# Performance work log

Hardware: AMD Instinct MI355X
Metric: run time of the kernel (lower is better)

## Reference

```python
import jax, jax.numpy as jnp
import numpy as np

N_WAY, N_SHOT = 10, 15
N_QUERY, D = 8192, 1024
C_REG = 0.1
MAX_ITER = 15


def setup_inputs() -> dict:
    key = jax.random.key(0)
    k1, k2 = jax.random.split(key)
    n_sup = N_WAY * N_SHOT
    feat = jax.random.normal(k1, (n_sup + N_QUERY, D), dtype=jnp.float32) * 0.1
    label_support = jnp.arange(N_WAY, dtype=jnp.int32)
    label_query = jax.random.randint(k2, (N_QUERY,), 0, N_WAY, dtype=jnp.int32)
    scale = jnp.ones((1,), dtype=jnp.float32)
    return {"feat": feat, "label_support": label_support,
            "label_query": label_query, "scale": scale}


def _qp_solve(Q, p, h, A):
    """min 0.5 z'Qz + p'z  s.t.  z <= h,  A z = 0.
    Infeasible-start primal-dual interior-point method, MAX_ITER fixed iterations
    (mirrors qpth's QPFunction(maxIter=15) iterative batched-solve structure)."""
    n = Q.shape[0]
    m = A.shape[0]
    dtype = Q.dtype
    z = h - 1.0                      # slack s = h - z = 1 > 0
    s = jnp.ones((n,), dtype)
    lam = jnp.ones((n,), dtype)
    nu = jnp.zeros((m,), dtype)
    sigma = jnp.asarray(0.1, dtype)  # centering parameter

    def step(carry, _):
        z, s, lam, nu = carry
        mu = jnp.dot(s, lam) / n
        rd = Q @ z + p + lam + A.T @ nu      # dual residual
        rp = A @ z                           # primal (equality) residual, b = 0
        rc = s * lam - sigma * mu            # complementarity residual
        r1 = -rd + rc / s
        H = Q + jnp.diag(lam / s)
        L = jnp.linalg.cholesky(H)
        solveH = lambda r: jax.scipy.linalg.cho_solve((L, True), r)
        Hinv_AT = solveH(A.T)                # (n, m)
        Hinv_r1 = solveH(r1)                 # (n,)
        S = A @ Hinv_AT                      # (m, m) Schur complement
        dnu = jnp.linalg.solve(S, A @ Hinv_r1 + rp)
        dz = Hinv_r1 - Hinv_AT @ dnu
        ds = -dz
        dlam = (lam * dz - rc) / s

        def max_step(v, dv):                 # largest alpha keeping v + alpha*dv > 0
            ratios = jnp.where(dv < 0, -v / jnp.where(dv < 0, dv, -1.0), jnp.inf)
            return jnp.min(ratios)

        alpha = jnp.minimum(1.0, 0.99 * jnp.minimum(max_step(s, ds), max_step(lam, dlam)))
        return (z + alpha * dz, s + alpha * ds, lam + alpha * dlam, nu + alpha * dnu), None

    (z, s, lam, nu), _ = jax.lax.scan(step, (z, s, lam, nu), None, length=MAX_ITER)
    return z


def reference(feat, label_support, label_query, scale):
    n_way, n_shot = N_WAY, N_SHOT
    n_sup = n_way * n_shot
    support = feat[:n_sup]                       # (n_sup, d)
    query = feat[n_sup:]                         # (n_q, d)
    sup_labels = jnp.repeat(label_support, n_shot)   # label[0].repeat_interleave(n_shot)

    K = support @ support.T                      # Gram matrix (n_sup, n_sup)
    n = n_sup * n_way
    eye_w = jnp.eye(n_way, dtype=K.dtype)
    # batched_kronecker(K, I_way): index (i*n_way + a)
    Q = jnp.einsum('ij,ab->iajb', K, eye_w).reshape(n, n) + 10.0 * jnp.eye(n, dtype=K.dtype)
    y_onehot = jax.nn.one_hot(sup_labels, n_way, dtype=K.dtype).reshape(n)
    p = -y_onehot                                # e
    h = C_REG * y_onehot                         # box: z <= C_reg * Y (C = I)
    # A = kron(I_{n_sup}, ones(1, n_way))
    A = jnp.einsum('ij,a->ija', jnp.eye(n_sup, dtype=K.dtype),
                   jnp.ones((n_way,), K.dtype)).reshape(n_sup, n)

    qp_sol = _qp_solve(Q, p, h, A).reshape(n_sup, n_way)

    compat = support @ query.T                   # (n_sup, n_q)
    # logits[q, w] = sum_s compat[s, q] * qp_sol[s, w]
    logits = scale[0] * jnp.einsum('sq,sw->qw', compat, qp_sol)
    log_prb = jax.nn.log_softmax(logits, axis=1)     # (n_q, n_way)
    y_q = jax.nn.one_hot(label_query, n_way, dtype=log_prb.dtype)
    loss = -(y_q * log_prb).sum(axis=1).mean()
    return (log_prb, loss)
```

## Files before the change

kernel.cpp:

```cpp
#include <hip/hip_runtime.h>


#define NW    10
#define NSH   15
#define NSUP  150
#define NQ    8192
#define DIM   1024
#define NVAR  1500
#define NP    152
#define NTT   19
#define NACT  (NTT*NTT)
#define TPB   384
#define SIGMA 0.1f
#define PSTR  68

#define OFF_K     0
#define OFF_Z     22800
#define OFF_S     24300
#define OFF_LAM   25800
#define OFF_NU    27300
#define OFF_R1    27452
#define OFF_DZ    28952
#define OFF_DLAM  30452
#define OFF_DNU   31952
#define OFF_RP    32104
#define OFF_MU    32256
#define OFF_ALPHA 32257
#define OFF_LP    32260
#define OFF_WT    34308
#define OFF_G     44548
#define OFF_SMAT  46048
#define OFF_X     69152
#define XSZ       (NP*NP)

__device__ __forceinline__ void bgj_invert(float (&H)[8][8], const int t, const int tr, const int tc,
                                           float (*rowbuf)[PSTR], float (*colbuf)[PSTR],
                                           float (*wbuf)[PSTR], float* pivinv) {
  const bool act = (t < NACT);
  const int r8 = t & 7;
  const int wj = t >> 3;
  for (int kb = 0; kb < NTT; ++kb) {
    if (act && tr == kb) {
      float4* dst = (float4*)(&rowbuf[tc][0]);
#pragma unroll
      for (int r = 0; r < 8; ++r) {
        dst[2*r]   = make_float4(H[r][0],H[r][1],H[r][2],H[r][3]);
        dst[2*r+1] = make_float4(H[r][4],H[r][5],H[r][6],H[r][7]);
      }
    }
    if (act && tc == kb) {
      float4* dst = (float4*)(&colbuf[tr][0]);
#pragma unroll
      for (int r = 0; r < 8; ++r) {
        dst[2*r]   = make_float4(H[r][0],H[r][1],H[r][2],H[r][3]);
        dst[2*r+1] = make_float4(H[r][4],H[r][5],H[r][6],H[r][7]);
      }
    }
    __syncthreads();
    if (t < 64) {
      const int r = t >> 3, c = t & 7;
      float p = rowbuf[kb][t];
#pragma unroll
      for (int pp = 0; pp < 8; ++pp) {
        const float pv   = __shfl(p, pp*9, 64);
        const float d    = 1.0f / pv;
        const float rowv = __shfl(p, pp*8 + c, 64);
        const float colv = __shfl(p, r*8 + pp, 64);
        const float nr   = rowv * d;
        float v = fmaf(-colv, nr, p);
        if (r == pp) v = nr;
        if (c == pp) v = -colv * d;
        if (r == pp && c == pp) v = d;
        p = v;
      }
      pivinv[t] = p;
    }
    __syncthreads();
    if (t < 8*NTT) {
      float w[8];
      if (wj == kb) {
#pragma unroll
        for (int c = 0; c < 8; ++c) w[c] = pivinv[r8*8+c];
      } else {
        const float4* rs = (const float4*)(&rowbuf[wj][0]);
#pragma unroll
        for (int c = 0; c < 8; ++c) w[c] = 0.0f;
#pragma unroll
        for (int q = 0; q < 8; ++q) {
          const float pq = pivinv[r8*8+q];
          const float4 x = rs[2*q], y = rs[2*q+1];
          w[0]=fmaf(pq,x.x,w[0]); w[1]=fmaf(pq,x.y,w[1]); w[2]=fmaf(pq,x.z,w[2]); w[3]=fmaf(pq,x.w,w[3]);
          w[4]=fmaf(pq,y.x,w[4]); w[5]=fmaf(pq,y.y,w[5]); w[6]=fmaf(pq,y.z,w[6]); w[7]=fmaf(pq,y.w,w[7]);
        }
      }
      float4* wd = (float4*)(&wbuf[wj][0]);
      wd[2*r8]   = make_float4(w[0],w[1],w[2],w[3]);
      wd[2*r8+1] = make_float4(w[4],w[5],w[6],w[7]);
    }
    __syncthreads();
    if (act) {
      if (tr == kb) {
        const float4* wsrc = (const float4*)(&wbuf[tc][0]);
#pragma unroll
        for (int r = 0; r < 8; ++r) {
          const float4 x = wsrc[2*r], y = wsrc[2*r+1];
          H[r][0]=x.x; H[r][1]=x.y; H[r][2]=x.z; H[r][3]=x.w;
          H[r][4]=y.x; H[r][5]=y.y; H[r][6]=y.z; H[r][7]=y.w;
        }
      } else {
        float C[8][8];
        const float4* cs = (const float4*)(&colbuf[tr][0]);
#pragma unroll
        for (int r = 0; r < 8; ++r) {
          const float4 x = cs[2*r], y = cs[2*r+1];
          C[r][0]=x.x; C[r][1]=x.y; C[r][2]=x.z; C[r][3]=x.w;
          C[r][4]=y.x; C[r][5]=y.y; C[r][6]=y.z; C[r][7]=y.w;
        }
        if (tc == kb) {
#pragma unroll
          for (int r = 0; r < 8; ++r)
#pragma unroll
            for (int c = 0; c < 8; ++c) H[r][c] = 0.0f;
        }
        const float4* wsrc = (const float4*)(&wbuf[tc][0]);
#pragma unroll
        for (int q = 0; q < 8; ++q) {
          const float4 x = wsrc[2*q], y = wsrc[2*q+1];
          const float w0=x.x,w1=x.y,w2=x.z,w3=x.w,w4=y.x,w5=y.y,w6=y.z,w7=y.w;
#pragma unroll
          for (int r = 0; r < 8; ++r) {
            const float cq = C[r][q];
            H[r][0]=fmaf(-cq,w0,H[r][0]); H[r][1]=fmaf(-cq,w1,H[r][1]);
            H[r][2]=fmaf(-cq,w2,H[r][2]); H[r][3]=fmaf(-cq,w3,H[r][3]);
            H[r][4]=fmaf(-cq,w4,H[r][4]); H[r][5]=fmaf(-cq,w5,H[r][5]);
            H[r][6]=fmaf(-cq,w6,H[r][6]); H[r][7]=fmaf(-cq,w7,H[r][7]);
          }
        }
      }
    }
    __syncthreads();
  }
}

__global__ __launch_bounds__(256) void k_gram(const float* __restrict__ feat, float* __restrict__ ws) {
  const int bi = blockIdx.x / 10, bj = blockIdx.x % 10;
  const int t = threadIdx.x;
  const int r = t / 15, c = t % 15;
  const bool act = (t < 225);
  __shared__ float As[15][65], Bs[15][65];
  float acc = 0.0f;
  for (int ch = 0; ch < 16; ++ch) {
    for (int idx = t; idx < 960; idx += 256) {
      const int rr = idx >> 6, dd = idx & 63;
      As[rr][dd] = feat[(bi*15+rr)*DIM + ch*64 + dd];
      Bs[rr][dd] = feat[(bj*15+rr)*DIM + ch*64 + dd];
    }
    __syncthreads();
    if (act) {
      for (int dd = 0; dd < 64; ++dd) acc += As[r][dd] * Bs[c][dd];
    }
    __syncthreads();
  }
  if (act) ws[OFF_K + (bi*15+r)*NP + (bj*15+c)] = acc;
}

__global__ __launch_bounds__(1024) void kinit(const int* __restrict__ labSup, float* __restrict__ ws) {
  const int t = threadIdx.x;
  for (int idx = t; idx < NVAR; idx += 1024) {
    const int i = idx / NW, aa = idx % NW;
    const float y = (labSup[i/NSH] == aa) ? 1.0f : 0.0f;
    ws[OFF_Z+idx]   = 0.1f*y - 1.0f;
    ws[OFF_S+idx]   = 1.0f;
    ws[OFF_LAM+idx] = 1.0f;
  }
  if (t < NP) ws[OFF_NU + t] = 0.0f;
  if (t == 0) ws[OFF_MU] = 1.0f;
  if (t < NSUP) {
    float rpv = 0.0f;
    for (int aa = 0; aa < NW; ++aa) {
      const float y = (labSup[t/NSH] == aa) ? 1.0f : 0.0f;
      rpv += 0.1f*y - 1.0f;
    }
    ws[OFF_RP + t] = rpv;
  }
}

__global__ __launch_bounds__(TPB, 2) void kqp1(const int* __restrict__ labSup, float* __restrict__ ws) {
  const int a = blockIdx.x;
  const int t = threadIdx.x;
  const int tr = t / NTT, tc = t % NTT;
  const bool act = (t < NACT);
  __shared__ __align__(16) float rowbuf[NTT][PSTR], colbuf[NTT][PSTR], wbuf[NTT][PSTR];
  __shared__ __align__(16) float pivinv[64];
  __shared__ float zloc[NP], dloc[NP], r1loc[NP];
  __shared__ float pacc[NP][NTT];
  const float mu = ws[OFF_MU];
  for (int i = t; i < NP; i += TPB) {
    if (i < NSUP) {
      zloc[i] = ws[OFF_Z + i*NW + a];
      dloc[i] = ws[OFF_LAM + i*NW + a] / ws[OFF_S + i*NW + a];
    } else { zloc[i] = 0.0f; dloc[i] = 0.0f; }
  }
  __syncthreads();
  float H[8][8];
  if (act) {
#pragma unroll
    for (int r = 0; r < 8; ++r) {
      const int row = 8*tr + r;
      if (row < NSUP) {
        const float4* ks = (const float4*)(ws + OFF_K + row*NP + 8*tc);
        const float4 x = ks[0], y = ks[1];
        H[r][0]=x.x; H[r][1]=x.y; H[r][2]=x.z; H[r][3]=x.w;
        H[r][4]=y.x; H[r][5]=y.y; H[r][6]=y.z; H[r][7]=y.w;
        if (tc == NTT-1) { H[r][6] = 0.0f; H[r][7] = 0.0f; }
      } else {
#pragma unroll
        for (int c = 0; c < 8; ++c) H[r][c] = 0.0f;
      }
#pragma unroll
      for (int c = 0; c < 8; ++c) {
        const int col = 8*tc + c;
        if (col == row) H[r][c] += (row < NSUP) ? (10.0f + dloc[row]) : 1.0f;
      }
    }
#pragma unroll
    for (int r = 0; r < 8; ++r) {
      float p = 0.0f;
#pragma unroll
      for (int c = 0; c < 8; ++c) p = fmaf(H[r][c], zloc[8*tc + c], p);
      pacc[8*tr + r][tc] = p;
    }
  }
  __syncthreads();
  if (t < NSUP) {
    float hz = 0.0f;
    for (int q = 0; q < NTT; ++q) hz += pacc[t][q];
    const float qz  = hz - dloc[t]*zloc[t];
    const float y   = (labSup[t/NSH] == a) ? 1.0f : 0.0f;
    const float svv = ws[OFF_S + t*NW+a], lvv = ws[OFF_LAM + t*NW+a];
    const float rd  = qz - y + lvv + ws[OFF_NU + t];
    const float rc  = svv*lvv - SIGMA*mu;
    const float r1v = -rd + rc/svv;
    ws[OFF_R1 + t*NW+a] = r1v;
    r1loc[t] = r1v;
  }
  if (t >= NSUP && t < NP) r1loc[t] = 0.0f;
  bgj_invert(H, t, tr, tc, rowbuf, colbuf, wbuf, pivinv);
  if (act) {
    float* Xa = ws + OFF_X + a*XSZ;
#pragma unroll
    for (int r = 0; r < 8; ++r) {
      float4* dst = (float4*)(Xa + (8*tr+r)*NP + 8*tc);
      dst[0] = make_float4(H[r][0],H[r][1],H[r][2],H[r][3]);
      dst[1] = make_float4(H[r][4],H[r][5],H[r][6],H[r][7]);
    }
#pragma unroll
    for (int r = 0; r < 8; ++r) {
      float p = 0.0f;
#pragma unroll
      for (int c = 0; c < 8; ++c) p = fmaf(H[r][c], r1loc[8*tc+c], p);
      pacc[8*tr+r][tc] = p;
    }
  }
  __syncthreads();
  if (t < NSUP) {
    float g = 0.0f;
    for (int q = 0; q < NTT; ++q) g += pacc[t][q];
    ws[OFF_G + t*NW + a] = g;
  }
}

__global__ __launch_bounds__(256) void k_sum(float* __restrict__ ws) {
  for (int idx = blockIdx.x*256 + threadIdx.x; idx < XSZ; idx += gridDim.x*256) {
    float v = 0.0f;
#pragma unroll
    for (int a = 0; a < NW; ++a) v += ws[OFF_X + a*XSZ + idx];
    ws[OFF_SMAT + idx] = v;
  }
}

__global__ __launch_bounds__(TPB, 2) void kqp2(float* __restrict__ ws) {
  const int t = threadIdx.x;
  const int tr = t / NTT, tc = t % NTT;
  const bool act = (t < NACT);
  __shared__ __align__(16) float rowbuf[NTT][PSTR], colbuf[NTT][PSTR], wbuf[NTT][PSTR];
  __shared__ __align__(16) float pivinv[64];
  __shared__ float tloc[NP];
  __shared__ float pacc[NP][NTT];
  float Sg[8][8];
  if (act) {
#pragma unroll
    for (int r = 0; r < 8; ++r) {
      const float4* ss = (const float4*)(ws + OFF_SMAT + (8*tr+r)*NP + 8*tc);
      const float4 x = ss[0], y = ss[1];
      Sg[r][0]=x.x; Sg[r][1]=x.y; Sg[r][2]=x.z; Sg[r][3]=x.w;
      Sg[r][4]=y.x; Sg[r][5]=y.y; Sg[r][6]=y.z; Sg[r][7]=y.w;
    }
  }
  if (t < NP) {
    float v = 0.0f;
    if (t < NSUP) {
      v = ws[OFF_RP + t];
#pragma unroll
      for (int a = 0; a < NW; ++a) v += ws[OFF_G + t*NW + a];
    }
    tloc[t] = v;
  }
  bgj_invert(Sg, t, tr, tc, rowbuf, colbuf, wbuf, pivinv);
  if (act) {
#pragma unroll
    for (int r = 0; r < 8; ++r) {
      float p = 0.0f;
#pragma unroll
      for (int c = 0; c < 8; ++c) p = fmaf(Sg[r][c], tloc[8*tc+c], p);
      pacc[8*tr+r][tc] = p;
    }
  }
  __syncthreads();
  if (t < NP) {
    float v = 0.0f;
    if (t < NSUP) for (int q = 0; q < NTT; ++q) v += pacc[t][q];
    ws[OFF_DNU + t] = v;
  }
  if (t == 0) ((unsigned*)ws)[OFF_ALPHA] = 0x7F800000u;
}

__global__ __launch_bounds__(TPB) void kqp3(float* __restrict__ ws) {
  const int a = blockIdx.x;
  const int t = threadIdx.x;
  const int tr = t / NTT, tc = t % NTT;
  const bool act = (t < NACT);
  __shared__ float vloc[NP];
  __shared__ float pacc[NP][NTT];
  const float mu = ws[OFF_MU];
  for (int i = t; i < NP; i += TPB)
    vloc[i] = (i < NSUP) ? (ws[OFF_R1 + i*NW + a] - ws[OFF_DNU + i]) : 0.0f;
  __syncthreads();
  if (act) {
    const float* Xa = ws + OFF_X + a*XSZ;
    const int cb = 8*tc;
#pragma unroll
    for (int r = 0; r < 8; ++r) {
      const float4* src = (const float4*)(Xa + (8*tr+r)*NP + cb);
      const float4 v0 = src[0], v1 = src[1];
      pacc[8*tr+r][tc] =
          v0.x*vloc[cb+0] + v0.y*vloc[cb+1] + v0.z*vloc[cb+2] + v0.w*vloc[cb+3]
        + v1.x*vloc[cb+4] + v1.y*vloc[cb+5] + v1.z*vloc[cb+6] + v1.w*vloc[cb+7];
    }
  }
  __syncthreads();
  if (t < NSUP) {
    float dzv = 0.0f;
    for (int q = 0; q < NTT; ++q) dzv += pacc[t][q];
    const float svv = ws[OFF_S + t*NW+a], lvv = ws[OFF_LAM + t*NW+a];
    const float rc  = svv*lvv - SIGMA*mu;
    const float dlv = (lvv*dzv - rc)/svv;
    ws[OFF_DZ + t*NW+a]   = dzv;
    ws[OFF_DLAM + t*NW+a] = dlv;
    unsigned* slot = (unsigned*)(ws) + OFF_ALPHA;
    const float dsv = -dzv;
    if (dsv < 0.0f) atomicMin(slot, __float_as_uint(-svv/dsv));
    if (dlv < 0.0f) atomicMin(slot, __float_as_uint(-lvv/dlv));
  }
}

__global__ __launch_bounds__(1024) void kqp4(float* __restrict__ ws) {
  const int t = threadIdx.x;
  __shared__ float zsh[NVAR];
  __shared__ float red[1024];
  const float am = __uint_as_float(((unsigned*)ws)[OFF_ALPHA]);
  const float alpha = fminf(1.0f, 0.99f * am);
  float part = 0.0f;
  for (int idx = t; idx < NVAR; idx += 1024) {
    const float dzv = ws[OFF_DZ + idx], dlv = ws[OFF_DLAM + idx];
    const float zn = ws[OFF_Z + idx]   + alpha*dzv;
    const float sn = ws[OFF_S + idx]   - alpha*dzv;
    const float ln = ws[OFF_LAM + idx] + alpha*dlv;
    ws[OFF_Z+idx]=zn; ws[OFF_S+idx]=sn; ws[OFF_LAM+idx]=ln;
    zsh[idx] = zn;
    part += sn*ln;
  }
  if (t < NSUP) ws[OFF_NU + t] += alpha * ws[OFF_DNU + t];
  red[t] = part;
  __syncthreads();
  for (int off = 512; off > 0; off >>= 1) {
    if (t < off) red[t] += red[t + off];
    __syncthreads();
  }
  if (t == 0) ws[OFF_MU] = red[0] / (float)NVAR;
  if (t < NSUP) {
    float rpv = 0.0f;
#pragma unroll
    for (int a = 0; a < NW; ++a) rpv += zsh[t*NW+a];
    ws[OFF_RP + t] = rpv;
  }
}

__global__ __launch_bounds__(1024) void k_wt(const float* __restrict__ feat,
                                             const float* __restrict__ scale,
                                             float* __restrict__ ws) {
  const int w = blockIdx.x;
  const int dd = threadIdx.x;
  float acc = 0.0f;
  for (int ss = 0; ss < NSUP; ++ss)
    acc += feat[ss*DIM + dd] * ws[OFF_Z + ss*NW + w];
  ws[OFF_WT + w*DIM + dd] = acc * scale[0];
}

__global__ __launch_bounds__(256) void k_logits(const float* __restrict__ feat,
                                                const int* __restrict__ labq,
                                                float* __restrict__ out,
                                                float* __restrict__ ws) {
  const int t = threadIdx.x;
  const int wv = t >> 6, l = t & 63;
  const int q = blockIdx.x*4 + wv;
  __shared__ float wtl[NW][DIM];
  __shared__ float lpart[4];
  for (int idx = t; idx < NW*DIM; idx += 256) wtl[idx >> 10][idx & 1023] = ws[OFF_WT + idx];
  __syncthreads();
  const float* qrow = feat + (size_t)(NSUP + q)*DIM;
  float acc[NW];
#pragma unroll
  for (int w = 0; w < NW; ++w) acc[w] = 0.0f;
#pragma unroll
  for (int c = 0; c < 4; ++c) {
    const float4 qv = *(const float4*)(qrow + c*256 + 4*l);
#pragma unroll
    for (int w = 0; w < NW; ++w) {
      const float4 wvv = *(const float4*)(&wtl[w][c*256 + 4*l]);
      acc[w] += qv.x*wvv.x + qv.y*wvv.y + qv.z*wvv.z + qv.w*wvv.w;
    }
  }
#pragma unroll
  for (int w = 0; w < NW; ++w) {
#pragma unroll
    for (int off = 32; off > 0; off >>= 1)
      acc[w] += __shfl_xor(acc[w], off, 64);
  }
  float m = acc[0];
#pragma unroll
  for (int w = 1; w < NW; ++w) m = fmaxf(m, acc[w]);
  float se = 0.0f;
#pragma unroll
  for (int w = 0; w < NW; ++w) se += expf(acc[w]-m);
  const float lse = m + logf(se);
  const int y = labq[q];
  if (l == 0) {
    float lpy = 0.0f;
#pragma unroll
    for (int w = 0; w < NW; ++w) {
      const float lp = acc[w] - lse;
      out[q*NW + w] = lp;
      if (w == y) lpy = lp;
    }
    lpart[wv] = -lpy;
  }
  __syncthreads();
  if (t == 0) ws[OFF_LP + blockIdx.x] = lpart[0]+lpart[1]+lpart[2]+lpart[3];
}

__global__ __launch_bounds__(1024) void k_loss(float* __restrict__ out, const float* __restrict__ ws) {
  const int t = threadIdx.x;
  __shared__ float red[1024];
  red[t] = ws[OFF_LP + t] + ws[OFF_LP + 1024 + t];
  __syncthreads();
  for (int off = 512; off > 0; off >>= 1) {
    if (t < off) red[t] += red[t + off];
    __syncthreads();
  }
  if (t == 0) out[NQ*NW] = red[0] / (float)NQ;
}

extern "C" void kernel_launch(void* const* d_in, const int* in_sizes, int n_in,
                              void* d_out, int out_size, void* d_ws, size_t ws_size,
                              hipStream_t stream) {
  const float* feat  = (const float*)d_in[0];
  const int*   labS  = (const int*)d_in[1];
  const int*   labQ  = (const int*)d_in[2];
  const float* scale = (const float*)d_in[3];
  float* ws  = (float*)d_ws;
  float* out = (float*)d_out;

  k_gram<<<100, 256, 0, stream>>>(feat, ws);
  kinit<<<1, 1024, 0, stream>>>(labS, ws);
  for (int it = 0; it < 15; ++it) {
    kqp1<<<NW, TPB, 0, stream>>>(labS, ws);
    k_sum<<<32, 256, 0, stream>>>(ws);
    kqp2<<<1,  TPB, 0, stream>>>(ws);
    kqp3<<<NW, TPB, 0, stream>>>(ws);
    kqp4<<<1, 1024, 0, stream>>>(ws);
  }
  k_wt<<<NW, 1024, 0, stream>>>(feat, scale, ws);
  k_logits<<<NQ/4, 256, 0, stream>>>(feat, labQ, out, ws);
  k_loss<<<1, 1024, 0, stream>>>(out, ws);
}
```

Measured before the change: 2.167 ms.

## Fuse QP solve steps into one kernel and cut barriers in block inversion

The per-iteration kernels kqp2, kqp3 and kqp4 are merged into a single one-block kernel. It computes dnu, loops over the ten classes to form dz and dlam, takes alpha through a shared-memory atomic min, and applies the update with a wave-shuffle reduction. This removes two launches per iteration, 30 in total. The block Gauss-Jordan inversion is restructured so every wave redundantly inverts the pivot block via shuffles, and the next pivot row and column are staged at the end of the current step into a double-buffered colbuf. That cuts the barriers per pivot step from four to two. The trade-off is that kqp3's ten-block parallel work now runs serially in one block.

```diff
diff --git a/kernel.cpp b/kernel.cpp
--- a/kernel.cpp
+++ b/kernel.cpp
@@ -22,10 +22,8 @@
 #define OFF_R1    27452
 #define OFF_DZ    28952
 #define OFF_DLAM  30452
-#define OFF_DNU   31952
 #define OFF_RP    32104
 #define OFF_MU    32256
-#define OFF_ALPHA 32257
 #define OFF_LP    32260
 #define OFF_WT    34308
 #define OFF_G     44548
@@ -33,69 +31,51 @@
 #define OFF_X     69152
 #define XSZ       (NP*NP)
 
-__device__ __forceinline__ void bgj_invert(float (&H)[8][8], const int t, const int tr, const int tc,
-                                           float (*rowbuf)[PSTR], float (*colbuf)[PSTR],
-                                           float (*wbuf)[PSTR], float* pivinv) {
+__device__ __forceinline__ void bgj_core(float (&H)[8][8], const int t, const int tr, const int tc,
+                                         float (*rowbuf)[PSTR], float (*colbuf)[NTT][PSTR],
+                                         float (*wbuf)[PSTR]) {
+  const int lane = t & 63;
+  const int pr = lane >> 3, pc = lane & 7;
+  const int r8 = t & 7;
+  const int wj2 = t >> 3;
+  const int jb = wj2 >> 1;
+  const int jh4 = (wj2 & 1) << 2;
+  const bool wact = (t < 8*NTT*2);
   const bool act = (t < NACT);
-  const int r8 = t & 7;
-  const int wj = t >> 3;
   for (int kb = 0; kb < NTT; ++kb) {
-    if (act && tr == kb) {
-      float4* dst = (float4*)(&rowbuf[tc][0]);
-#pragma unroll
-      for (int r = 0; r < 8; ++r) {
-        dst[2*r]   = make_float4(H[r][0],H[r][1],H[r][2],H[r][3]);
-        dst[2*r+1] = make_float4(H[r][4],H[r][5],H[r][6],H[r][7]);
-      }
-    }
-    if (act && tc == kb) {
-      float4* dst = (float4*)(&colbuf[tr][0]);
-#pragma unroll
-      for (int r = 0; r < 8; ++r) {
-        dst[2*r]   = make_float4(H[r][0],H[r][1],H[r][2],H[r][3]);
-        dst[2*r+1] = make_float4(H[r][4],H[r][5],H[r][6],H[r][7]);
-      }
-    }
-    __syncthreads();
-    if (t < 64) {
-      const int r = t >> 3, c = t & 7;
-      float p = rowbuf[kb][t];
-#pragma unroll
-      for (int pp = 0; pp < 8; ++pp) {
-        const float pv   = __shfl(p, pp*9, 64);
-        const float d    = 1.0f / pv;
-        const float rowv = __shfl(p, pp*8 + c, 64);
-        const float colv = __shfl(p, r*8 + pp, 64);
-        const float nr   = rowv * d;
-        float v = fmaf(-colv, nr, p);
-        if (r == pp) v = nr;
-        if (c == pp) v = -colv * d;
-        if (r == pp && c == pp) v = d;
-        p = v;
-      }
-      pivinv[t] = p;
-    }
-    __syncthreads();
-    if (t < 8*NTT) {
-      float w[8];
-      if (wj == kb) {
-#pragma unroll
-        for (int c = 0; c < 8; ++c) w[c] = pivinv[r8*8+c];
+    const int cur = kb & 1, nxt = cur ^ 1;
+    float p = rowbuf[kb][lane];
+#pragma unroll
+    for (int pp = 0; pp < 8; ++pp) {
+      const float pv   = __shfl(p, pp*9, 64);
+      const float d    = 1.0f / pv;
+      const float rowv = __shfl(p, pp*8 + pc, 64);
+      const float colv = __shfl(p, pr*8 + pp, 64);
+      const float nr   = rowv * d;
+      float v = fmaf(-colv, nr, p);
+      if (pr == pp) v = nr;
+      if (pc == pp) v = -colv * d;
+      if (pr == pp && pc == pp) v = d;
+      p = v;
+    }
+    float pv8[8];
+#pragma unroll
+    for (int q = 0; q < 8; ++q) pv8[q] = __shfl(p, r8*8 + q, 64);
+    if (wact) {
+      float w0, w1, w2, w3;
+      if (jb == kb) {
+        w0 = jh4 ? pv8[4] : pv8[0]; w1 = jh4 ? pv8[5] : pv8[1];
+        w2 = jh4 ? pv8[6] : pv8[2]; w3 = jh4 ? pv8[7] : pv8[3];
       } else {
-        const float4* rs = (const float4*)(&rowbuf[wj][0]);
-#pragma unroll
-        for (int c = 0; c < 8; ++c) w[c] = 0.0f;
+        w0 = w1 = w2 = w3 = 0.0f;
 #pragma unroll
         for (int q = 0; q < 8; ++q) {
-          const float pq = pivinv[r8*8+q];
-          const float4 x = rs[2*q], y = rs[2*q+1];
-          w[0]=fmaf(pq,x.x,w[0]); w[1]=fmaf(pq,x.y,w[1]); w[2]=fmaf(pq,x.z,w[2]); w[3]=fmaf(pq,x.w,w[3]);
-          w[4]=fmaf(pq,y.x,w[4]); w[5]=fmaf(pq,y.y,w[5]); w[6]=fmaf(pq,y.z,w[6]); w[7]=fmaf(pq,y.w,w[7]);
-        }
-      }
-      float4* wd = (float4*)(&wbuf[wj][0]);
-      wd[2*r8]   = make_float4(w[0],w[1],w[2],w[3]);
-      wd[2*r8+1] = make_float4(w[4],w[5],w[6],w[7]);
+          const float4 x = *(const float4*)(&rowbuf[jb][q*8 + jh4]);
+          w0 = fmaf(pv8[q], x.x, w0); w1 = fmaf(pv8[q], x.y, w1);
+          w2 = fmaf(pv8[q], x.z, w2); w3 = fmaf(pv8[q], x.w, w3);
+        }
+      }
+      *(float4*)(&wbuf[jb][r8*8 + jh4]) = make_float4(w0, w1, w2, w3);
     }
     __syncthreads();
     if (act) {
@@ -109,7 +89,7 @@
         }
       } else {
         float C[8][8];
-        const float4* cs = (const float4*)(&colbuf[tr][0]);
+        const float4* cs = (const float4*)(&colbuf[cur][tr][0]);
 #pragma unroll
         for (int r = 0; r < 8; ++r) {
           const float4 x = cs[2*r], y = cs[2*r+1];
@@ -134,6 +114,24 @@
             H[r][2]=fmaf(-cq,w2,H[r][2]); H[r][3]=fmaf(-cq,w3,H[r][3]);
             H[r][4]=fmaf(-cq,w4,H[r][4]); H[r][5]=fmaf(-cq,w5,H[r][5]);
             H[r][6]=fmaf(-cq,w6,H[r][6]); H[r][7]=fmaf(-cq,w7,H[r][7]);
+          }
+        }
+      }
+      if (kb < NTT-1) {
+        if (tr == kb+1) {
+          float4* dst = (float4*)(&rowbuf[tc][0]);
+#pragma unroll
+          for (int r = 0; r < 8; ++r) {
+            dst[2*r]   = make_float4(H[r][0],H[r][1],H[r][2],H[r][3]);
+            dst[2*r+1] = make_float4(H[r][4],H[r][5],H[r][6],H[r][7]);
+          }
+        }
+        if (tc == kb+1) {
+          float4* dst = (float4*)(&colbuf[nxt][tr][0]);
+#pragma unroll
+          for (int r = 0; r < 8; ++r) {
+            dst[2*r]   = make_float4(H[r][0],H[r][1],H[r][2],H[r][3]);
+            dst[2*r+1] = make_float4(H[r][4],H[r][5],H[r][6],H[r][7]);
           }
         }
       }
@@ -185,13 +183,12 @@
   }
 }
 
-__global__ __launch_bounds__(TPB, 2) void kqp1(const int* __restrict__ labSup, float* __restrict__ ws) {
+__global__ __launch_bounds__(TPB, 2) void kqpA(const int* __restrict__ labSup, float* __restrict__ ws) {
   const int a = blockIdx.x;
   const int t = threadIdx.x;
   const int tr = t / NTT, tc = t % NTT;
   const bool act = (t < NACT);
-  __shared__ __align__(16) float rowbuf[NTT][PSTR], colbuf[NTT][PSTR], wbuf[NTT][PSTR];
-  __shared__ __align__(16) float pivinv[64];
+  __shared__ __align__(16) float rowbuf[NTT][PSTR], colbuf[2][NTT][PSTR], wbuf[NTT][PSTR];
   __shared__ float zloc[NP], dloc[NP], r1loc[NP];
   __shared__ float pacc[NP][NTT];
   const float mu = ws[OFF_MU];
@@ -229,6 +226,22 @@
 #pragma unroll
       for (int c = 0; c < 8; ++c) p = fmaf(H[r][c], zloc[8*tc + c], p);
       pacc[8*tr + r][tc] = p;
+    }
+    if (tr == 0) {
+      float4* dst = (float4*)(&rowbuf[tc][0]);
+#pragma unroll
+      for (int r = 0; r < 8; ++r) {
+        dst[2*r]   = make_float4(H[r][0],H[r][1],H[r][2],H[r][3]);
+        dst[2*r+1] = make_float4(H[r][4],H[r][5],H[r][6],H[r][7]);
+      }
+    }
+    if (tc == 0) {
+      float4* dst = (float4*)(&colbuf[0][tr][0]);
+#pragma unroll
+      for (int r = 0; r < 8; ++r) {
+        dst[2*r]   = make_float4(H[r][0],H[r][1],H[r][2],H[r][3]);
+        dst[2*r+1] = make_float4(H[r][4],H[r][5],H[r][6],H[r][7]);
+      }
     }
   }
   __syncthreads();
@@ -243,9 +256,8 @@
     const float r1v = -rd + rc/svv;
     ws[OFF_R1 + t*NW+a] = r1v;
     r1loc[t] = r1v;
-  }
-  if (t >= NSUP && t < NP) r1loc[t] = 0.0f;
-  bgj_invert(H, t, tr, tc, rowbuf, colbuf, wbuf, pivinv);
+  } else if (t < NP) r1loc[t] = 0.0f;
+  bgj_core(H, t, tr, tc, rowbuf, colbuf, wbuf);
   if (act) {
     float* Xa = ws + OFF_X + a*XSZ;
 #pragma unroll
@@ -279,14 +291,27 @@
   }
 }
 
-__global__ __launch_bounds__(TPB, 2) void kqp2(float* __restrict__ ws) {
+__global__ __launch_bounds__(TPB, 2) void kqpB(float* __restrict__ ws) {
   const int t = threadIdx.x;
   const int tr = t / NTT, tc = t % NTT;
   const bool act = (t < NACT);
-  __shared__ __align__(16) float rowbuf[NTT][PSTR], colbuf[NTT][PSTR], wbuf[NTT][PSTR];
-  __shared__ __align__(16) float pivinv[64];
-  __shared__ float tloc[NP];
+  __shared__ __align__(16) float rowbuf[NTT][PSTR], colbuf[2][NTT][PSTR], wbuf[NTT][PSTR];
+  __shared__ float tloc[NP], dnuloc[NP], vloc[NP];
   __shared__ float pacc[NP][NTT];
+  __shared__ float zsh[NVAR];
+  __shared__ float wred[TPB/64];
+  __shared__ unsigned alphaU;
+  const float mu = ws[OFF_MU];
+  if (t == 0) alphaU = 0x7F800000u;
+  if (t < NP) {
+    float v = 0.0f;
+    if (t < NSUP) {
+      v = ws[OFF_RP + t];
+#pragma unroll
+      for (int a = 0; a < NW; ++a) v += ws[OFF_G + t*NW + a];
+    }
+    tloc[t] = v;
+  }
   float Sg[8][8];
   if (act) {
 #pragma unroll
@@ -296,17 +321,25 @@
       Sg[r][0]=x.x; Sg[r][1]=x.y; Sg[r][2]=x.z; Sg[r][3]=x.w;
       Sg[r][4]=y.x; Sg[r][5]=y.y; Sg[r][6]=y.z; Sg[r][7]=y.w;
     }
-  }
-  if (t < NP) {
-    float v = 0.0f;
-    if (t < NSUP) {
-      v = ws[OFF_RP + t];
-#pragma unroll
-      for (int a = 0; a < NW; ++a) v += ws[OFF_G + t*NW + a];
-    }
-    tloc[t] = v;
-  }
-  bgj_invert(Sg, t, tr, tc, rowbuf, colbuf, wbuf, pivinv);
+    if (tr == 0) {
+      float4* dst = (float4*)(&rowbuf[tc][0]);
+#pragma unroll
+      for (int r = 0; r < 8; ++r) {
+        dst[2*r]   = make_float4(Sg[r][0],Sg[r][1],Sg[r][2],Sg[r][3]);
+        dst[2*r+1] = make_float4(Sg[r][4],Sg[r][5],Sg[r][6],Sg[r][7]);
+      }
+    }
+    if (tc == 0) {
+      float4* dst = (float4*)(&colbuf[0][tr][0]);
+#pragma unroll
+      for (int r = 0; r < 8; ++r) {
+        dst[2*r]   = make_float4(Sg[r][0],Sg[r][1],Sg[r][2],Sg[r][3]);
+        dst[2*r+1] = make_float4(Sg[r][4],Sg[r][5],Sg[r][6],Sg[r][7]);
+      }
+    }
+  }
+  __syncthreads();
+  bgj_core(Sg, t, tr, tc, rowbuf, colbuf, wbuf);
   if (act) {
 #pragma unroll
     for (int r = 0; r < 8; ++r) {
@@ -320,58 +353,43 @@
   if (t < NP) {
     float v = 0.0f;
     if (t < NSUP) for (int q = 0; q < NTT; ++q) v += pacc[t][q];
-    ws[OFF_DNU + t] = v;
-  }
-  if (t == 0) ((unsigned*)ws)[OFF_ALPHA] = 0x7F800000u;
-}
-
-__global__ __launch_bounds__(TPB) void kqp3(float* __restrict__ ws) {
-  const int a = blockIdx.x;
-  const int t = threadIdx.x;
-  const int tr = t / NTT, tc = t % NTT;
-  const bool act = (t < NACT);
-  __shared__ float vloc[NP];
-  __shared__ float pacc[NP][NTT];
-  const float mu = ws[OFF_MU];
-  for (int i = t; i < NP; i += TPB)
-    vloc[i] = (i < NSUP) ? (ws[OFF_R1 + i*NW + a] - ws[OFF_DNU + i]) : 0.0f;
-  __syncthreads();
-  if (act) {
-    const float* Xa = ws + OFF_X + a*XSZ;
-    const int cb = 8*tc;
-#pragma unroll
-    for (int r = 0; r < 8; ++r) {
-      const float4* src = (const float4*)(Xa + (8*tr+r)*NP + cb);
-      const float4 v0 = src[0], v1 = src[1];
-      pacc[8*tr+r][tc] =
-          v0.x*vloc[cb+0] + v0.y*vloc[cb+1] + v0.z*vloc[cb+2] + v0.w*vloc[cb+3]
-        + v1.x*vloc[cb+4] + v1.y*vloc[cb+5] + v1.z*vloc[cb+6] + v1.w*vloc[cb+7];
-    }
-  }
-  __syncthreads();
-  if (t < NSUP) {
-    float dzv = 0.0f;
-    for (int q = 0; q < NTT; ++q) dzv += pacc[t][q];
-    const float svv = ws[OFF_S + t*NW+a], lvv = ws[OFF_LAM + t*NW+a];
-    const float rc  = svv*lvv - SIGMA*mu;
-    const float dlv = (lvv*dzv - rc)/svv;
-    ws[OFF_DZ + t*NW+a]   = dzv;
-    ws[OFF_DLAM + t*NW+a] = dlv;
-    unsigned* slot = (unsigned*)(ws) + OFF_ALPHA;
-    const float dsv = -dzv;
-    if (dsv < 0.0f) atomicMin(slot, __float_as_uint(-svv/dsv));
-    if (dlv < 0.0f) atomicMin(slot, __float_as_uint(-lvv/dlv));
-  }
-}
-
-__global__ __launch_bounds__(1024) void kqp4(float* __restrict__ ws) {
-  const int t = threadIdx.x;
-  __shared__ float zsh[NVAR];
-  __shared__ float red[1024];
-  const float am = __uint_as_float(((unsigned*)ws)[OFF_ALPHA]);
-  const float alpha = fminf(1.0f, 0.99f * am);
+    dnuloc[t] = v;
+  }
+  __syncthreads();
+  for (int a = 0; a < NW; ++a) {
+    for (int i = t; i < NP; i += TPB)
+      vloc[i] = (i < NSUP) ? (ws[OFF_R1 + i*NW + a] - dnuloc[i]) : 0.0f;
+    __syncthreads();
+    if (act) {
+      const float* Xa = ws + OFF_X + a*XSZ;
+      const int cb = 8*tc;
+#pragma unroll
+      for (int r = 0; r < 8; ++r) {
+        const float4* src = (const float4*)(Xa + (8*tr+r)*NP + cb);
+        const float4 v0 = src[0], v1 = src[1];
+        pacc[8*tr+r][tc] =
+            v0.x*vloc[cb+0] + v0.y*vloc[cb+1] + v0.z*vloc[cb+2] + v0.w*vloc[cb+3]
+          + v1.x*vloc[cb+4] + v1.y*vloc[cb+5] + v1.z*vloc[cb+6] + v1.w*vloc[cb+7];
+      }
+    }
+    __syncthreads();
+    if (t < NSUP) {
+      float dzv = 0.0f;
+      for (int q = 0; q < NTT; ++q) dzv += pacc[t][q];
+      const float svv = ws[OFF_S + t*NW+a], lvv = ws[OFF_LAM + t*NW+a];
+      const float rc  = svv*lvv - SIGMA*mu;
+      const float dlv = (lvv*dzv - rc)/svv;
+      ws[OFF_DZ + t*NW+a]   = dzv;
+      ws[OFF_DLAM + t*NW+a] = dlv;
+      const float dsv = -dzv;
+      if (dsv < 0.0f) atomicMin(&alphaU, __float_as_uint(-svv/dsv));
+      if (dlv < 0.0f) atomicMin(&alphaU, __float_as_uint(-lvv/dlv));
+    }
+    __syncthreads();
+  }
+  const float alpha = fminf(1.0f, 0.99f * __uint_as_float(alphaU));
   float part = 0.0f;
-  for (int idx = t; idx < NVAR; idx += 1024) {
+  for (int idx = t; idx < NVAR; idx += TPB) {
     const float dzv = ws[OFF_DZ + idx], dlv = ws[OFF_DLAM + idx];
     const float zn = ws[OFF_Z + idx]   + alpha*dzv;
     const float sn = ws[OFF_S + idx]   - alpha*dzv;
@@ -380,14 +398,17 @@
     zsh[idx] = zn;
     part += sn*ln;
   }
-  if (t < NSUP) ws[OFF_NU + t] += alpha * ws[OFF_DNU + t];
-  red[t] = part;
-  __syncthreads();
-  for (int off = 512; off > 0; off >>= 1) {
-    if (t < off) red[t] += red[t + off];
-    __syncthreads();
-  }
-  if (t == 0) ws[OFF_MU] = red[0] / (float)NVAR;
+  if (t < NSUP) ws[OFF_NU + t] += alpha * dnuloc[t];
+#pragma unroll
+  for (int off = 32; off > 0; off >>= 1) part += __shfl_xor(part, off, 64);
+  if ((t & 63) == 0) wred[t >> 6] = part;
+  __syncthreads();
+  if (t == 0) {
+    float s = 0.0f;
+#pragma unroll
+    for (int wv = 0; wv < TPB/64; ++wv) s += wred[wv];
+    ws[OFF_MU] = s / (float)NVAR;
+  }
   if (t < NSUP) {
     float rpv = 0.0f;
 #pragma unroll
@@ -484,11 +505,9 @@
   k_gram<<<100, 256, 0, stream>>>(feat, ws);
   kinit<<<1, 1024, 0, stream>>>(labS, ws);
   for (int it = 0; it < 15; ++it) {
-    kqp1<<<NW, TPB, 0, stream>>>(labS, ws);
+    kqpA<<<NW, TPB, 0, stream>>>(labS, ws);
     k_sum<<<32, 256, 0, stream>>>(ws);
-    kqp2<<<1,  TPB, 0, stream>>>(ws);
-    kqp3<<<NW, TPB, 0, stream>>>(ws);
-    kqp4<<<1, 1024, 0, stream>>>(ws);
+    kqpB<<<1, TPB, 0, stream>>>(ws);
   }
   k_wt<<<NW, 1024, 0, stream>>>(feat, scale, ws);
   k_logits<<<NQ/4, 256, 0, stream>>>(feat, labQ, out, ws);
```

Result: slower. 2.818 ms (+30.0%).

## Rework block Gauss-Jordan inversion to 4x8 tiles with double-buffered panels

Applied to the files above, without the earlier changes.

Splits the 152x152 inversion across 722 threads holding 4x8 register tiles instead of 361 threads holding 8x8, doubling the threads per block. Each wave now recomputes the 8x8 pivot inverse redundantly via shuffles, removing the shared pivinv buffer and one barrier per step. The next step's pivot row and column panels are written at the end of each step, with the column panel stored transposed and double-buffered, cutting the barriers per step from four to two. The cost is higher per-thread redundant pivot work and more shared-memory traffic per FMA in the smaller tiles.

```diff
diff --git a/kernel.cpp b/kernel.cpp
--- a/kernel.cpp
+++ b/kernel.cpp
@@ -8,11 +8,16 @@
 #define DIM   1024
 #define NVAR  1500
 #define NP    152
+#define CB    19
+#define RB    38
+#define NACT2 722
+#define TPB2  768
+#define TPB   384
 #define NTT   19
 #define NACT  (NTT*NTT)
-#define TPB   384
 #define SIGMA 0.1f
 #define PSTR  68
+#define CTSTR 36
 
 #define OFF_K     0
 #define OFF_Z     22800
@@ -33,108 +38,95 @@
 #define OFF_X     69152
 #define XSZ       (NP*NP)
 
-__device__ __forceinline__ void bgj_invert(float (&H)[8][8], const int t, const int tr, const int tc,
-                                           float (*rowbuf)[PSTR], float (*colbuf)[PSTR],
-                                           float (*wbuf)[PSTR], float* pivinv) {
-  const bool act = (t < NACT);
-  const int r8 = t & 7;
-  const int wj = t >> 3;
-  for (int kb = 0; kb < NTT; ++kb) {
-    if (act && tr == kb) {
-      float4* dst = (float4*)(&rowbuf[tc][0]);
-#pragma unroll
-      for (int r = 0; r < 8; ++r) {
-        dst[2*r]   = make_float4(H[r][0],H[r][1],H[r][2],H[r][3]);
-        dst[2*r+1] = make_float4(H[r][4],H[r][5],H[r][6],H[r][7]);
-      }
-    }
-    if (act && tc == kb) {
-      float4* dst = (float4*)(&colbuf[tr][0]);
-#pragma unroll
-      for (int r = 0; r < 8; ++r) {
-        dst[2*r]   = make_float4(H[r][0],H[r][1],H[r][2],H[r][3]);
-        dst[2*r+1] = make_float4(H[r][4],H[r][5],H[r][6],H[r][7]);
-      }
-    }
-    __syncthreads();
-    if (t < 64) {
-      const int r = t >> 3, c = t & 7;
-      float p = rowbuf[kb][t];
-#pragma unroll
-      for (int pp = 0; pp < 8; ++pp) {
-        const float pv   = __shfl(p, pp*9, 64);
-        const float d    = 1.0f / pv;
-        const float rowv = __shfl(p, pp*8 + c, 64);
-        const float colv = __shfl(p, r*8 + pp, 64);
-        const float nr   = rowv * d;
-        float v = fmaf(-colv, nr, p);
-        if (r == pp) v = nr;
-        if (c == pp) v = -colv * d;
-        if (r == pp && c == pp) v = d;
-        p = v;
-      }
-      pivinv[t] = p;
-    }
-    __syncthreads();
-    if (t < 8*NTT) {
-      float w[8];
-      if (wj == kb) {
-#pragma unroll
-        for (int c = 0; c < 8; ++c) w[c] = pivinv[r8*8+c];
-      } else {
-        const float4* rs = (const float4*)(&rowbuf[wj][0]);
-#pragma unroll
-        for (int c = 0; c < 8; ++c) w[c] = 0.0f;
+__device__ __forceinline__ void bgj48(float (&H)[4][8], const int t, const int trb, const int tcb,
+                                      float (*rowbuf)[PSTR], float (*colbufT)[RB][CTSTR],
+                                      float (*wbuf)[PSTR]) {
+  const int lane = t & 63;
+  const int pr = lane >> 3, pc = lane & 7;
+  const int wr  = t & 7;
+  const int wcp = t >> 3;
+  const int wcb = wcp >> 2;
+  const int wc2 = (wcp & 3) * 2;
+  const bool wact = (t < 608);
+  const bool act  = (t < NACT2);
+  for (int kb = 0; kb < CB; ++kb) {
+    const int cur = kb & 1, nxt = cur ^ 1;
+    float p = rowbuf[kb][lane];
+#pragma unroll
+    for (int pp = 0; pp < 8; ++pp) {
+      const float pv   = __shfl(p, pp*9, 64);
+      const float d    = 1.0f / pv;
+      const float rowv = __shfl(p, pp*8 + pc, 64);
+      const float colv = __shfl(p, pr*8 + pp, 64);
+      const float nr   = rowv * d;
+      float v = fmaf(-colv, nr, p);
+      if (pr == pp) v = nr;
+      if (pc == pp) v = -colv * d;
+      if (pr == pp && pc == pp) v = d;
+      p = v;
+    }
+    float pv8[8];
+#pragma unroll
+    for (int q = 0; q < 8; ++q) pv8[q] = __shfl(p, wr*8 + q, 64);
+    if (wact) {
+      float w0, w1;
+      if (wcb == kb) { w0 = pv8[wc2]; w1 = pv8[wc2+1]; }
+      else {
+        w0 = w1 = 0.0f;
 #pragma unroll
         for (int q = 0; q < 8; ++q) {
-          const float pq = pivinv[r8*8+q];
-          const float4 x = rs[2*q], y = rs[2*q+1];
-          w[0]=fmaf(pq,x.x,w[0]); w[1]=fmaf(pq,x.y,w[1]); w[2]=fmaf(pq,x.z,w[2]); w[3]=fmaf(pq,x.w,w[3]);
-          w[4]=fmaf(pq,y.x,w[4]); w[5]=fmaf(pq,y.y,w[5]); w[6]=fmaf(pq,y.z,w[6]); w[7]=fmaf(pq,y.w,w[7]);
+          const float2 rv = *(const float2*)(&rowbuf[wcb][q*8 + wc2]);
+          w0 = fmaf(pv8[q], rv.x, w0);
+          w1 = fmaf(pv8[q], rv.y, w1);
         }
       }
-      float4* wd = (float4*)(&wbuf[wj][0]);
-      wd[2*r8]   = make_float4(w[0],w[1],w[2],w[3]);
-      wd[2*r8+1] = make_float4(w[4],w[5],w[6],w[7]);
+      *(float2*)(&wbuf[wcb][wr*8 + wc2]) = make_float2(w0, w1);
     }
     __syncthreads();
     if (act) {
-      if (tr == kb) {
-        const float4* wsrc = (const float4*)(&wbuf[tc][0]);
-#pragma unroll
-        for (int r = 0; r < 8; ++r) {
-          const float4 x = wsrc[2*r], y = wsrc[2*r+1];
+      if ((trb >> 1) == kb) {
+        const int rbase = (trb & 1) * 4;
+#pragma unroll
+        for (int r = 0; r < 4; ++r) {
+          const float4 x = *(const float4*)(&wbuf[tcb][(rbase+r)*8]);
+          const float4 y = *(const float4*)(&wbuf[tcb][(rbase+r)*8+4]);
           H[r][0]=x.x; H[r][1]=x.y; H[r][2]=x.z; H[r][3]=x.w;
           H[r][4]=y.x; H[r][5]=y.y; H[r][6]=y.z; H[r][7]=y.w;
         }
       } else {
-        float C[8][8];
-        const float4* cs = (const float4*)(&colbuf[tr][0]);
-#pragma unroll
-        for (int r = 0; r < 8; ++r) {
-          const float4 x = cs[2*r], y = cs[2*r+1];
-          C[r][0]=x.x; C[r][1]=x.y; C[r][2]=x.z; C[r][3]=x.w;
-          C[r][4]=y.x; C[r][5]=y.y; C[r][6]=y.z; C[r][7]=y.w;
-        }
-        if (tc == kb) {
-#pragma unroll
-          for (int r = 0; r < 8; ++r)
+        if (tcb == kb) {
+#pragma unroll
+          for (int r = 0; r < 4; ++r)
 #pragma unroll
             for (int c = 0; c < 8; ++c) H[r][c] = 0.0f;
         }
-        const float4* wsrc = (const float4*)(&wbuf[tc][0]);
 #pragma unroll
         for (int q = 0; q < 8; ++q) {
-          const float4 x = wsrc[2*q], y = wsrc[2*q+1];
-          const float w0=x.x,w1=x.y,w2=x.z,w3=x.w,w4=y.x,w5=y.y,w6=y.z,w7=y.w;
-#pragma unroll
-          for (int r = 0; r < 8; ++r) {
-            const float cq = C[r][q];
-            H[r][0]=fmaf(-cq,w0,H[r][0]); H[r][1]=fmaf(-cq,w1,H[r][1]);
-            H[r][2]=fmaf(-cq,w2,H[r][2]); H[r][3]=fmaf(-cq,w3,H[r][3]);
-            H[r][4]=fmaf(-cq,w4,H[r][4]); H[r][5]=fmaf(-cq,w5,H[r][5]);
-            H[r][6]=fmaf(-cq,w6,H[r][6]); H[r][7]=fmaf(-cq,w7,H[r][7]);
+          const float4 cq = *(const float4*)(&colbufT[cur][trb][q*4]);
+          const float4 wx = *(const float4*)(&wbuf[tcb][q*8]);
+          const float4 wy = *(const float4*)(&wbuf[tcb][q*8+4]);
+          const float cr[4] = {cq.x, cq.y, cq.z, cq.w};
+          const float wv[8] = {wx.x,wx.y,wx.z,wx.w,wy.x,wy.y,wy.z,wy.w};
+#pragma unroll
+          for (int r = 0; r < 4; ++r)
+#pragma unroll
+            for (int c = 0; c < 8; ++c)
+              H[r][c] = fmaf(-cr[r], wv[c], H[r][c]);
+        }
+      }
+      if (kb < CB-1) {
+        if ((trb >> 1) == kb+1) {
+          const int rbase = (trb & 1) * 4;
+#pragma unroll
+          for (int r = 0; r < 4; ++r) {
+            *(float4*)(&rowbuf[tcb][(rbase+r)*8])   = make_float4(H[r][0],H[r][1],H[r][2],H[r][3]);
+            *(float4*)(&rowbuf[tcb][(rbase+r)*8+4]) = make_float4(H[r][4],H[r][5],H[r][6],H[r][7]);
           }
+        }
+        if (tcb == kb+1) {
+#pragma unroll
+          for (int c = 0; c < 8; ++c)
+            *(float4*)(&colbufT[nxt][trb][c*4]) = make_float4(H[0][c],H[1][c],H[2][c],H[3][c]);
         }
       }
     }
@@ -185,56 +177,69 @@
   }
 }
 
-__global__ __launch_bounds__(TPB, 2) void kqp1(const int* __restrict__ labSup, float* __restrict__ ws) {
+__global__ __launch_bounds__(TPB2, 3) void kqpA(const int* __restrict__ labSup, float* __restrict__ ws) {
   const int a = blockIdx.x;
   const int t = threadIdx.x;
-  const int tr = t / NTT, tc = t % NTT;
-  const bool act = (t < NACT);
-  __shared__ __align__(16) float rowbuf[NTT][PSTR], colbuf[NTT][PSTR], wbuf[NTT][PSTR];
-  __shared__ __align__(16) float pivinv[64];
+  const int trb = t / CB, tcb = t % CB;
+  const bool act = (t < NACT2);
+  __shared__ __align__(16) float rowbuf[CB][PSTR], wbuf[CB][PSTR];
+  __shared__ __align__(16) float colbufT[2][RB][CTSTR];
   __shared__ float zloc[NP], dloc[NP], r1loc[NP];
-  __shared__ float pacc[NP][NTT];
+  __shared__ float pacc[NP][20];
   const float mu = ws[OFF_MU];
-  for (int i = t; i < NP; i += TPB) {
+  for (int i = t; i < NP; i += TPB2) {
     if (i < NSUP) {
       zloc[i] = ws[OFF_Z + i*NW + a];
       dloc[i] = ws[OFF_LAM + i*NW + a] / ws[OFF_S + i*NW + a];
     } else { zloc[i] = 0.0f; dloc[i] = 0.0f; }
   }
   __syncthreads();
-  float H[8][8];
+  float H[4][8];
   if (act) {
 #pragma unroll
-    for (int r = 0; r < 8; ++r) {
-      const int row = 8*tr + r;
+    for (int r = 0; r < 4; ++r) {
+      const int row = 4*trb + r;
       if (row < NSUP) {
-        const float4* ks = (const float4*)(ws + OFF_K + row*NP + 8*tc);
+        const float4* ks = (const float4*)(ws + OFF_K + row*NP + 8*tcb);
         const float4 x = ks[0], y = ks[1];
         H[r][0]=x.x; H[r][1]=x.y; H[r][2]=x.z; H[r][3]=x.w;
         H[r][4]=y.x; H[r][5]=y.y; H[r][6]=y.z; H[r][7]=y.w;
-        if (tc == NTT-1) { H[r][6] = 0.0f; H[r][7] = 0.0f; }
+        if (tcb == CB-1) { H[r][6] = 0.0f; H[r][7] = 0.0f; }
       } else {
 #pragma unroll
         for (int c = 0; c < 8; ++c) H[r][c] = 0.0f;
       }
 #pragma unroll
       for (int c = 0; c < 8; ++c) {
-        const int col = 8*tc + c;
+        const int col = 8*tcb + c;
         if (col == row) H[r][c] += (row < NSUP) ? (10.0f + dloc[row]) : 1.0f;
       }
     }
 #pragma unroll
-    for (int r = 0; r < 8; ++r) {
+    for (int r = 0; r < 4; ++r) {
       float p = 0.0f;
 #pragma unroll
-      for (int c = 0; c < 8; ++c) p = fmaf(H[r][c], zloc[8*tc + c], p);
-      pacc[8*tr + r][tc] = p;
+      for (int c = 0; c < 8; ++c) p = fmaf(H[r][c], zloc[8*tcb + c], p);
+      pacc[4*trb + r][tcb] = p;
+    }
+    if ((trb >> 1) == 0) {
+      const int rbase = (trb & 1) * 4;
+#pragma unroll
+      for (int r = 0; r < 4; ++r) {
+        *(float4*)(&rowbuf[tcb][(rbase+r)*8])   = make_float4(H[r][0],H[r][1],H[r][2],H[r][3]);
+        *(float4*)(&rowbuf[tcb][(rbase+r)*8+4]) = make_float4(H[r][4],H[r][5],H[r][6],H[r][7]);
+      }
+    }
+    if (tcb == 0) {
+#pragma unroll
+      for (int c = 0; c < 8; ++c)
+        *(float4*)(&colbufT[0][trb][c*4]) = make_float4(H[0][c],H[1][c],H[2][c],H[3][c]);
     }
   }
   __syncthreads();
   if (t < NSUP) {
     float hz = 0.0f;
-    for (int q = 0; q < NTT; ++q) hz += pacc[t][q];
+    for (int q = 0; q < CB; ++q) hz += pacc[t][q];
     const float qz  = hz - dloc[t]*zloc[t];
     const float y   = (labSup[t/NSH] == a) ? 1.0f : 0.0f;
     const float svv = ws[OFF_S + t*NW+a], lvv = ws[OFF_LAM + t*NW+a];
@@ -243,29 +248,28 @@
     const float r1v = -rd + rc/svv;
     ws[OFF_R1 + t*NW+a] = r1v;
     r1loc[t] = r1v;
-  }
-  if (t >= NSUP && t < NP) r1loc[t] = 0.0f;
-  bgj_invert(H, t, tr, tc, rowbuf, colbuf, wbuf, pivinv);
+  } else if (t < NP) r1loc[t] = 0.0f;
+  bgj48(H, t, trb, tcb, rowbuf, colbufT, wbuf);
   if (act) {
     float* Xa = ws + OFF_X + a*XSZ;
 #pragma unroll
-    for (int r = 0; r < 8; ++r) {
-      float4* dst = (float4*)(Xa + (8*tr+r)*NP + 8*tc);
+    for (int r = 0; r < 4; ++r) {
+      float4* dst = (float4*)(Xa + (4*trb+r)*NP + 8*tcb);
       dst[0] = make_float4(H[r][0],H[r][1],H[r][2],H[r][3]);
       dst[1] = make_float4(H[r][4],H[r][5],H[r][6],H[r][7]);
     }
 #pragma unroll
-    for (int r = 0; r < 8; ++r) {
+    for (int r = 0; r < 4; ++r) {
       float p = 0.0f;
 #pragma unroll
-      for (int c = 0; c < 8; ++c) p = fmaf(H[r][c], r1loc[8*tc+c], p);
-      pacc[8*tr+r][tc] = p;
+      for (int c = 0; c < 8; ++c) p = fmaf(H[r][c], r1loc[8*tcb+c], p);
+      pacc[4*trb+r][tcb] = p;
     }
   }
   __syncthreads();
   if (t < NSUP) {
     float g = 0.0f;
-    for (int q = 0; q < NTT; ++q) g += pacc[t][q];
+    for (int q = 0; q < CB; ++q) g += pacc[t][q];
     ws[OFF_G + t*NW + a] = g;
   }
 }
@@ -279,24 +283,14 @@
   }
 }
 
-__global__ __launch_bounds__(TPB, 2) void kqp2(float* __restrict__ ws) {
-  const int t = threadIdx.x;
-  const int tr = t / NTT, tc = t % NTT;
-  const bool act = (t < NACT);
-  __shared__ __align__(16) float rowbuf[NTT][PSTR], colbuf[NTT][PSTR], wbuf[NTT][PSTR];
-  __shared__ __align__(16) float pivinv[64];
+__global__ __launch_bounds__(TPB2, 3) void kqpB(float* __restrict__ ws) {
+  const int t = threadIdx.x;
+  const int trb = t / CB, tcb = t % CB;
+  const bool act = (t < NACT2);
+  __shared__ __align__(16) float rowbuf[CB][PSTR], wbuf[CB][PSTR];
+  __shared__ __align__(16) float colbufT[2][RB][CTSTR];
   __shared__ float tloc[NP];
-  __shared__ float pacc[NP][NTT];
-  float Sg[8][8];
-  if (act) {
-#pragma unroll
-    for (int r = 0; r < 8; ++r) {
-      const float4* ss = (const float4*)(ws + OFF_SMAT + (8*tr+r)*NP + 8*tc);
-      const float4 x = ss[0], y = ss[1];
-      Sg[r][0]=x.x; Sg[r][1]=x.y; Sg[r][2]=x.z; Sg[r][3]=x.w;
-      Sg[r][4]=y.x; Sg[r][5]=y.y; Sg[r][6]=y.z; Sg[r][7]=y.w;
-    }
-  }
+  __shared__ float pacc[NP][20];
   if (t < NP) {
     float v = 0.0f;
     if (t < NSUP) {
@@ -306,20 +300,44 @@
     }
     tloc[t] = v;
   }
-  bgj_invert(Sg, t, tr, tc, rowbuf, colbuf, wbuf, pivinv);
+  float Sg[4][8];
   if (act) {
 #pragma unroll
-    for (int r = 0; r < 8; ++r) {
+    for (int r = 0; r < 4; ++r) {
+      const float4* ss = (const float4*)(ws + OFF_SMAT + (4*trb+r)*NP + 8*tcb);
+      const float4 x = ss[0], y = ss[1];
+      Sg[r][0]=x.x; Sg[r][1]=x.y; Sg[r][2]=x.z; Sg[r][3]=x.w;
+      Sg[r][4]=y.x; Sg[r][5]=y.y; Sg[r][6]=y.z; Sg[r][7]=y.w;
+    }
+    if ((trb >> 1) == 0) {
+      const int rbase = (trb & 1) * 4;
+#pragma unroll
+      for (int r = 0; r < 4; ++r) {
+        *(float4*)(&rowbuf[tcb][(rbase+r)*8])   = make_float4(Sg[r][0],Sg[r][1],Sg[r][2],Sg[r][3]);
+        *(float4*)(&rowbuf[tcb][(rbase+r)*8+4]) = make_float4(Sg[r][4],Sg[r][5],Sg[r][6],Sg[r][7]);
+      }
+    }
+    if (tcb == 0) {
+#pragma unroll
+      for (int c = 0; c < 8; ++c)
+        *(float4*)(&colbufT[0][trb][c*4]) = make_float4(Sg[0][c],Sg[1][c],Sg[2][c],Sg[3][c]);
+    }
+  }
+  __syncthreads();
+  bgj48(Sg, t, trb, tcb, rowbuf, colbufT, wbuf);
+  if (act) {
+#pragma unroll
+    for (int r = 0; r < 4; ++r) {
       float p = 0.0f;
 #pragma unroll
-      for (int c = 0; c < 8; ++c) p = fmaf(Sg[r][c], tloc[8*tc+c], p);
-      pacc[8*tr+r][tc] = p;
-    }
-  }
-  __syncthreads();
-  if (t < NP) {
+      for (int c = 0; c < 8; ++c) p = fmaf(Sg[r][c], tloc[8*tcb+c], p);
+      pacc[4*trb+r][tcb] = p;
+    }
+  }
+  __syncthreads();
+  if (t < NSUP) {
     float v = 0.0f;
-    if (t < NSUP) for (int q = 0; q < NTT; ++q) v += pacc[t][q];
+    for (int q = 0; q < CB; ++q) v += pacc[t][q];
     ws[OFF_DNU + t] = v;
   }
   if (t == 0) ((unsigned*)ws)[OFF_ALPHA] = 0x7F800000u;
@@ -484,9 +502,9 @@
   k_gram<<<100, 256, 0, stream>>>(feat, ws);
   kinit<<<1, 1024, 0, stream>>>(labS, ws);
   for (int it = 0; it < 15; ++it) {
-    kqp1<<<NW, TPB, 0, stream>>>(labS, ws);
+    kqpA<<<NW, TPB2, 0, stream>>>(labS, ws);
     k_sum<<<32, 256, 0, stream>>>(ws);
-    kqp2<<<1,  TPB, 0, stream>>>(ws);
+    kqpB<<<1, TPB2, 0, stream>>>(ws);
     kqp3<<<NW, TPB, 0, stream>>>(ws);
     kqp4<<<1, 1024, 0, stream>>>(ws);
   }
```

Result: no change. 2.174 ms (+0.3%).
